# Performance work log

Measured on AMD Instinct MI355X. Metric: run time of the kernel, lower is better.

The kernel has to match this reference:

```python
import jax, jax.numpy as jnp
import numpy as np

NUM_TYPES = 200
TOK_DIM = 10000
SMALL_DIM = 64
IN_DIM = 32 + 32 + SMALL_DIM  # 128
NUM_EDGE_TYPES = 3
STEPS = 4
BLOCKS = 2
PROJ_DIM = 128
N_NODES = 100000
N_EDGES = 600000
N_GRAPHS = 64


def setup_inputs() -> dict:
    key = jax.random.key(0)
    ks = jax.random.split(key, 20)
    s = 0.05
    inp = {
        'x_type': jax.random.randint(ks[0], (N_NODES,), 0, NUM_TYPES),
        'x_tok': jax.random.randint(ks[1], (N_NODES,), 0, TOK_DIM + 1),
        'x_small': jax.random.normal(ks[2], (N_NODES, SMALL_DIM), jnp.float32),
        'edge_index': jax.random.randint(ks[3], (2, N_EDGES), 0, N_NODES),
        'edge_type': jax.random.randint(ks[4], (N_EDGES,), 0, NUM_EDGE_TYPES),
        'batch': jnp.sort(jax.random.randint(ks[5], (N_NODES,), 0, N_GRAPHS)),
        # learned params
        'type_emb': jax.random.normal(ks[6], (NUM_TYPES, 32), jnp.float32),
        'tok_emb': jax.random.normal(ks[7], (TOK_DIM + 1, 32), jnp.float32),
        'msg_W': jax.random.normal(ks[8], (NUM_EDGE_TYPES, IN_DIM, IN_DIM), jnp.float32) * s,
        'msg_b': jax.random.normal(ks[9], (NUM_EDGE_TYPES, IN_DIM), jnp.float32) * s,
        'W_ih': jax.random.normal(ks[10], (3 * IN_DIM, IN_DIM), jnp.float32) * s,
        'W_hh': jax.random.normal(ks[11], (3 * IN_DIM, IN_DIM), jnp.float32) * s,
        'b_ih': jax.random.normal(ks[12], (3 * IN_DIM,), jnp.float32) * s,
        'b_hh': jax.random.normal(ks[13], (3 * IN_DIM,), jnp.float32) * s,
        'proj_W1': jax.random.normal(ks[14], (PROJ_DIM, IN_DIM), jnp.float32) * s,
        'proj_b1': jax.random.normal(ks[15], (PROJ_DIM,), jnp.float32) * s,
        'proj_W2': jax.random.normal(ks[16], (1, PROJ_DIM), jnp.float32) * s,
        'proj_b2': jax.random.normal(ks[17], (1,), jnp.float32) * s,
    }
    return inp


def _gru_cell(m, h, W_ih, W_hh, b_ih, b_hh):
    # torch.nn.GRU single step
    gi = m @ W_ih.T + b_ih  # [N, 3H]
    gh = h @ W_hh.T + b_hh
    i_r, i_z, i_n = jnp.split(gi, 3, axis=-1)
    h_r, h_z, h_n = jnp.split(gh, 3, axis=-1)
    r = jax.nn.sigmoid(i_r + h_r)
    z = jax.nn.sigmoid(i_z + h_z)
    n = jnp.tanh(i_n + r * h_n)
    return (1.0 - z) * n + z * h


def reference(x_type, x_tok, x_small, edge_index, edge_type, batch,
              type_emb, tok_emb, msg_W, msg_b,
              W_ih, W_hh, b_ih, b_hh,
              proj_W1, proj_b1, proj_W2, proj_b2):
    n = x_type.shape[0]
    x = jnp.concatenate([type_emb[x_type], tok_emb[x_tok], x_small], axis=-1)  # [N, IN_DIM]
    src, dst = edge_index[0], edge_index[1]
    for _ in range(BLOCKS * STEPS):
        # transform every node once per edge type: [T, N, D]
        h_all = jnp.einsum('ni,toi->tno', x, msg_W) + msg_b[:, None, :]
        # per-edge message = typed linear of source node (gather)
        m = h_all[edge_type, src]  # [E, D]
        agg = jax.ops.segment_sum(m, dst, num_segments=n)  # summed over edge types too
        x = _gru_cell(agg, x, W_ih, W_hh, b_ih, b_hh)
    # global mean pool over graphs
    sums = jax.ops.segment_sum(x, batch, num_segments=N_GRAPHS)
    counts = jax.ops.segment_sum(jnp.ones((n,), x.dtype), batch, num_segments=N_GRAPHS)
    pooled = sums / jnp.maximum(counts, 1.0)[:, None]
    h = jax.nn.relu(pooled @ proj_W1.T + proj_b1)  # dropout = identity in eval
    logits = (h @ proj_W2.T + proj_b2).reshape(-1)
    return logits
```

## Files before the change

kernel.cpp:

```cpp
#include <hip/hip_runtime.h>
#include <stdint.h>


typedef _Float16 f16;
typedef _Float16 v8hf __attribute__((ext_vector_type(8)));
typedef _Float16 v2hf __attribute__((ext_vector_type(2)));
typedef float    v16f __attribute__((ext_vector_type(16)));

#define GI_F 147456
#define GH_F 49152

__device__ __forceinline__ float sigf(float a){
  return __fdividef(1.0f, 1.0f + __expf(-a));
}
__device__ __forceinline__ float tanhf_fast(float a){
  return 1.0f - __fdividef(2.0f, __expf(2.0f*a) + 1.0f);
}

__global__ void k_diag(float* out, int n, float v){
  int i = threadIdx.x; if(i<n) out[i] = v;
}

__global__ void k_embed(const int* __restrict__ xtype, const int* __restrict__ xtok,
                        const float* __restrict__ xsmall,
                        const float* __restrict__ temb, const float* __restrict__ kemb,
                        f16* __restrict__ xb, int N){
  int n = blockIdx.x; int j = threadIdx.x;
  if(n>=N) return;
  float v;
  if(j<32)       v = temb[xtype[n]*32 + j];
  else if(j<64)  v = kemb[xtok[n]*32 + (j-32)];
  else           v = xsmall[(size_t)n*64 + (j-64)];
  xb[(size_t)n*128 + j] = (f16)v;
}

__global__ void k_wcomb(const float* __restrict__ W_ih, const float* __restrict__ msg_W,
                        float* __restrict__ Wc){
  int i = blockIdx.x*256 + threadIdx.x;
  if(i >= 147456) return;
  int o2 = i/384, K = i%384;
  const float* wr = W_ih + o2*128;
  const float* mc = msg_W + (K>>7)*16384 + (K&127);
  float acc = 0.f;
  #pragma unroll 4
  for(int k2=0;k2<128;k2++) acc += wr[k2]*mc[k2*128];
  Wc[i] = acc;
}

__global__ void k_mbp(const float* __restrict__ W_ih, const float* __restrict__ msg_b,
                      float* __restrict__ mbp){
  int i = blockIdx.x*256 + threadIdx.x;
  if(i >= 1152) return;
  int t = i/384, o2 = i%384;
  const float* wr = W_ih + o2*128;
  const float* mb = msg_b + t*128;
  float acc = 0.f;
  #pragma unroll 4
  for(int k2=0;k2<128;k2++) acc += wr[k2]*mb[k2];
  mbp[i] = acc;
}

__global__ void k_wprep(const float* __restrict__ Wc, const float* __restrict__ W_hh,
                        f16* __restrict__ WpF){
  int i = blockIdx.x*256 + threadIdx.x;
  if(i >= GI_F + GH_F) return;
  float w; int lane, j;
  if(i < GI_F){
    int grp = i/512, rem = i%512;
    lane = rem/8; j = rem%8;
    int tile = grp/24, ks = grp%24;
    int n = tile*32 + (lane&31);
    int k = ks*16 + (lane>>5)*8 + j;
    w = Wc[n*384 + k];
  } else {
    int i2 = i - GI_F;
    int grp = i2/512, rem = i2%512;
    lane = rem/8; j = rem%8;
    int tile = grp/8, ks = grp%8;
    int n = tile*32 + (lane&31);
    int k = ks*16 + (lane>>5)*8 + j;
    w = W_hh[n*128 + k];
  }
  WpF[i] = (f16)w;
}

__global__ void k_hist3(const int* __restrict__ dst, const int* __restrict__ et,
                        int* __restrict__ deg3, int E){
  int e = blockIdx.x*blockDim.x + threadIdx.x;
  if(e<E) atomicAdd(&deg3[dst[e]*3 + et[e]], 1);
}

__global__ void k_scan1(const int* __restrict__ deg, int n, int* __restrict__ part, int* __restrict__ bsum){
  __shared__ int s[256];
  int t = threadIdx.x;
  int base = blockIdx.x*1024 + t*4;
  int v[4]; int sum=0;
  #pragma unroll
  for(int k=0;k<4;k++){ int i=base+k; int d=(i<n)?deg[i]:0; sum+=d; v[k]=sum; }
  s[t]=sum; __syncthreads();
  for(int off=1;off<256;off<<=1){
    int add = (t>=off)? s[t-off] : 0;
    __syncthreads();
    s[t]+=add;
    __syncthreads();
  }
  int excl = (t>0)? s[t-1] : 0;
  #pragma unroll
  for(int k=0;k<4;k++){ int i=base+k; if(i<n) part[i]=v[k]+excl; }
  if(t==255) bsum[blockIdx.x] = s[255];
}

__global__ void k_scan2(const int* __restrict__ bsum, int nb, int* __restrict__ carry){
  if(threadIdx.x==0 && blockIdx.x==0){
    int c=0;
    for(int b=0;b<nb;b++){ carry[b]=c; c+=bsum[b]; }
  }
}

__global__ void k_finalize(const int* __restrict__ part, const int* __restrict__ deg,
                           const int* __restrict__ carry, int n,
                           int* __restrict__ rowptr, int* __restrict__ cursor){
  int i = blockIdx.x*blockDim.x + threadIdx.x;
  if(i>=n) return;
  int incl = part[i] + carry[i>>10];
  rowptr[i+1] = incl;
  cursor[i] = incl - deg[i];
  if(i==0) rowptr[0]=0;
}

__global__ void k_fill3(const int* __restrict__ src, const int* __restrict__ dst,
                        const int* __restrict__ et, int* __restrict__ cursor,
                        int* __restrict__ pay, int E){
  int e = blockIdx.x*blockDim.x + threadIdx.x;
  if(e>=E) return;
  int pos = atomicAdd(&cursor[dst[e]*3 + et[e]], 1);
  pay[pos] = src[e];
}

__global__ void k_gather3_c(const f16* __restrict__ xb, const int* __restrict__ rp3,
                            const int* __restrict__ pay, f16* __restrict__ s, int N){
  int n = blockIdx.x*4 + (threadIdx.x>>6);
  if(n >= N) return;
  int lane = threadIdx.x & 63;
  int c = lane*2;
  int b = n*3;
  int lo = rp3[b], e0 = rp3[b+1], e1 = rp3[b+2], hi = rp3[b+3];
  float a0=0.f,b0=0.f,a1=0.f,b1=0.f,a2=0.f,b2=0.f;
  int len = hi - lo;
  int t1 = lo + len/3;
  int t2 = lo + (2*len)/3;
  int iA = lo, iB = t1, iC = t2;
  while(iA < t1 && iB < t2 && iC < hi){
    int pA = pay[iA], pB = pay[iB], pC = pay[iC];
    v2hf uA = *(const v2hf*)&xb[(size_t)pA*128 + c];
    v2hf uB = *(const v2hf*)&xb[(size_t)pB*128 + c];
    v2hf uC = *(const v2hf*)&xb[(size_t)pC*128 + c];
    float fA0=(float)uA[0], fA1=(float)uA[1];
    float fB0=(float)uB[0], fB1=(float)uB[1];
    float fC0=(float)uC[0], fC1=(float)uC[1];
    if(iA < e0)      { a0+=fA0; b0+=fA1; }
    else if(iA < e1) { a1+=fA0; b1+=fA1; }
    else             { a2+=fA0; b2+=fA1; }
    if(iB < e0)      { a0+=fB0; b0+=fB1; }
    else if(iB < e1) { a1+=fB0; b1+=fB1; }
    else             { a2+=fB0; b2+=fB1; }
    if(iC < e0)      { a0+=fC0; b0+=fC1; }
    else if(iC < e1) { a1+=fC0; b1+=fC1; }
    else             { a2+=fC0; b2+=fC1; }
    iA++; iB++; iC++;
  }
  for(; iA < t1; iA++){
    v2hf u = *(const v2hf*)&xb[(size_t)pay[iA]*128 + c];
    float f0=(float)u[0], f1=(float)u[1];
    if(iA < e0)      { a0+=f0; b0+=f1; }
    else if(iA < e1) { a1+=f0; b1+=f1; }
    else             { a2+=f0; b2+=f1; }
  }
  for(; iB < t2; iB++){
    v2hf u = *(const v2hf*)&xb[(size_t)pay[iB]*128 + c];
    float f0=(float)u[0], f1=(float)u[1];
    if(iB < e0)      { a0+=f0; b0+=f1; }
    else if(iB < e1) { a1+=f0; b1+=f1; }
    else             { a2+=f0; b2+=f1; }
  }
  for(; iC < hi; iC++){
    v2hf u = *(const v2hf*)&xb[(size_t)pay[iC]*128 + c];
    float f0=(float)u[0], f1=(float)u[1];
    if(iC < e0)      { a0+=f0; b0+=f1; }
    else if(iC < e1) { a1+=f0; b1+=f1; }
    else             { a2+=f0; b2+=f1; }
  }
  size_t o = (size_t)n*384 + c;
  v2hf t;
  t[0]=(f16)a0; t[1]=(f16)b0; *(v2hf*)&s[o]     = t;
  t[0]=(f16)a1; t[1]=(f16)b1; *(v2hf*)&s[o+128] = t;
  t[0]=(f16)a2; t[1]=(f16)b2; *(v2hf*)&s[o+256] = t;
}

#define SSTR 392
#define XSTR 136
__global__ __launch_bounds__(256,2) void k_mega2(
    const f16* __restrict__ xb_old, f16* __restrict__ xb_new,
    const f16* __restrict__ s, const f16* __restrict__ WpF,
    const int* __restrict__ deg3, const float* __restrict__ mbp,
    const float* __restrict__ b_ih, const float* __restrict__ b_hh, int M)
{
  __shared__ f16 Ss[32*SSTR];
  __shared__ f16 Ax[32*XSTR];
  __shared__ float Dg[96];
  int tid = threadIdx.x, lane = tid & 63, w = tid >> 6;
  int lrow = lane & 31, q = lane >> 5;
  int row0 = blockIdx.x * 32;

  #pragma unroll
  for(int p=0;p<2;p++){
    int ch = tid + p*256;
    int row = ch>>4, c8 = (ch&15)*8;
    int gr = row0 + row; if(gr >= M) gr = M-1;
    *(v8hf*)&Ax[row*XSTR + c8] = *(const v8hf*)(xb_old + (size_t)gr*128 + c8);
  }
  #pragma unroll
  for(int p=0;p<6;p++){
    int ch = tid + p*256;
    int row = ch/48, c8 = (ch%48)*8;
    int gr = row0 + row; if(gr >= M) gr = M-1;
    *(v8hf*)&Ss[row*SSTR + c8] = *(const v8hf*)(s + (size_t)gr*384 + c8);
  }
  if(tid < 96){
    int node = row0 + tid/3;
    Dg[tid] = (node < M) ? (float)deg3[node*3 + (tid - (tid/3)*3)] : 0.f;
  }
  __syncthreads();

  v16f agi[3] = {};
  #pragma unroll
  for(int ks=0; ks<24; ks++){
    int kb = ks*16 + q*8;
    v8hf a0 = *(const v8hf*)&Ss[lrow*SSTR + kb];
    #pragma unroll
    for(int ct=0; ct<3; ct++){
      int tile = ct*4 + w;
      v8hf bh = *(const v8hf*)(WpF + (size_t)(tile*24 + ks)*512 + lane*8);
      agi[ct] = __builtin_amdgcn_mfma_f32_32x32x16_f16(a0, bh, agi[ct], 0,0,0);
    }
  }
  v2hf gip[3][8];
  #pragma unroll
  for(int ct=0; ct<3; ct++)
    #pragma unroll
    for(int rp=0; rp<8; rp++){
      v2hf t; t[0] = (f16)agi[ct][2*rp]; t[1] = (f16)agi[ct][2*rp+1];
      gip[ct][rp] = t;
    }

  v16f agh[3] = {};
  #pragma unroll
  for(int ks=0; ks<8; ks++){
    int kb = ks*16 + q*8;
    v8hf a0 = *(const v8hf*)&Ax[lrow*XSTR + kb];
    #pragma unroll
    for(int ct=0; ct<3; ct++){
      int tile = ct*4 + w;
      v8hf bh = *(const v8hf*)(WpF + GI_F + (size_t)(tile*8 + ks)*512 + lane*8);
      agh[ct] = __builtin_amdgcn_mfma_f32_32x32x16_f16(a0, bh, agh[ct], 0,0,0);
    }
  }

  int jf = w*32 + lrow;
  float bi0 = b_ih[jf],     bh0 = b_hh[jf];
  float bi1 = b_ih[128+jf], bh1 = b_hh[128+jf];
  float bi2 = b_ih[256+jf], bh2 = b_hh[256+jf];
  float mb[3][3];
  #pragma unroll
  for(int t=0;t<3;t++){
    mb[t][0] = mbp[t*384 + jf];
    mb[t][1] = mbp[t*384 + 128 + jf];
    mb[t][2] = mbp[t*384 + 256 + jf];
  }
  int rq4 = 4*q;
  #pragma unroll
  for(int r=0;r<16;r++){
    int gl = (r&3) + 8*(r>>2) + rq4;
    float d0 = Dg[gl*3], d1 = Dg[gl*3+1], d2 = Dg[gl*3+2];
    float g0 = (float)gip[0][r>>1][r&1];
    float g1 = (float)gip[1][r>>1][r&1];
    float g2 = (float)gip[2][r>>1][r&1];
    float ir  = g0 + bi0 + d0*mb[0][0] + d1*mb[1][0] + d2*mb[2][0];
    float iz  = g1 + bi1 + d0*mb[0][1] + d1*mb[1][1] + d2*mb[2][1];
    float in_ = g2 + bi2 + d0*mb[0][2] + d1*mb[1][2] + d2*mb[2][2];
    float hr  = agh[0][r] + bh0;
    float hz  = agh[1][r] + bh1;
    float hn  = agh[2][r] + bh2;
    float rg = sigf(ir + hr);
    float zg = sigf(iz + hz);
    float nn = tanhf_fast(in_ + rg*hn);
    float xo = (float)Ax[gl*XSTR + jf];
    Ax[gl*XSTR + jf] = (f16)((1.f - zg)*nn + zg*xo);
  }
  __syncthreads();
  #pragma unroll
  for(int p=0;p<2;p++){
    int ch = tid + p*256;
    int row = ch>>4, c8 = (ch&15)*8;
    int gr = row0 + row;
    if(gr < M)
      *(v8hf*)(xb_new + (size_t)gr*128 + c8) = *(const v8hf*)&Ax[row*XSTR + c8];
  }
}

__device__ __forceinline__ int lb_batch(const int* __restrict__ batch, int N, int g){
  int lo=0, hi=N;
  while(lo<hi){ int mid=(lo+hi)>>1; if(batch[mid]<g) lo=mid+1; else hi=mid; }
  return lo;
}

__global__ void k_pool2(const f16* __restrict__ xb, const int* __restrict__ batch,
                        float* __restrict__ pooled, int N){
  int g = blockIdx.x, slice = blockIdx.y;
  int j = threadIdx.x;
  int lo = lb_batch(batch,N,g), hi = lb_batch(batch,N,g+1);
  float acc = 0.f;
  for(int r=lo+slice; r<hi; r+=32) acc += (float)xb[(size_t)r*128 + j];
  atomicAdd(&pooled[g*128+j], acc);
}

__global__ void k_head(const float* __restrict__ pooled, const int* __restrict__ batch, int N,
                       const float* __restrict__ W1, const float* __restrict__ b1,
                       const float* __restrict__ W2, const float* __restrict__ b2,
                       float* __restrict__ out){
  int g = blockIdx.x; int j = threadIdx.x;
  __shared__ float p[128];
  __shared__ float red[128];
  int lo = lb_batch(batch,N,g), hi = lb_batch(batch,N,g+1);
  float c = (float)(hi-lo); if(c < 1.f) c = 1.f;
  p[j] = pooled[g*128+j] / c;
  __syncthreads();
  float acc = b1[j];
  #pragma unroll 4
  for(int i=0;i<128;i++) acc += W1[j*128+i]*p[i];
  float v = (acc>0.f?acc:0.f) * W2[j];
  red[j] = v; __syncthreads();
  for(int s=64;s>0;s>>=1){ if(j<s) red[j]+=red[j+s]; __syncthreads(); }
  if(j==0) out[g] = red[0] + b2[0];
}

extern "C" void kernel_launch(void* const* d_in, const int* in_sizes, int n_in,
                              void* d_out, int out_size, void* d_ws, size_t ws_size,
                              hipStream_t stream){
  const int*   x_type    = (const int*)d_in[0];
  const int*   x_tok     = (const int*)d_in[1];
  const float* x_small   = (const float*)d_in[2];
  const int*   edge_index= (const int*)d_in[3];
  const int*   edge_type = (const int*)d_in[4];
  const int*   batch     = (const int*)d_in[5];
  const float* type_emb  = (const float*)d_in[6];
  const float* tok_emb   = (const float*)d_in[7];
  const float* msg_W     = (const float*)d_in[8];
  const float* msg_b     = (const float*)d_in[9];
  const float* W_ih      = (const float*)d_in[10];
  const float* W_hh      = (const float*)d_in[11];
  const float* b_ih      = (const float*)d_in[12];
  const float* b_hh      = (const float*)d_in[13];
  const float* pW1       = (const float*)d_in[14];
  const float* pb1       = (const float*)d_in[15];
  const float* pW2       = (const float*)d_in[16];
  const float* pb2       = (const float*)d_in[17];
  float* out = (float*)d_out;

  int N = in_sizes[0];
  int E = in_sizes[3]/2;
  const int* src = edge_index;
  const int* dst = edge_index + E;
  int n3 = 3*N;
  int nch = (n3+1023)/1024;

  char* w = (char*)d_ws;
  size_t off = 0;
  auto alloc = [&](size_t bytes)->char*{ char* p = w + off; off += (bytes + 511) & ~511ull; return p; };
  f16*   xb0    = (f16*)alloc((size_t)N*128*2);
  f16*   xb1    = (f16*)alloc((size_t)N*128*2);
  f16*   s      = (f16*)alloc((size_t)N*384*2);
  int*   deg3   = (int*)alloc((size_t)n3*4);
  int*   part   = (int*)alloc((size_t)n3*4);
  int*   rp3    = (int*)alloc((size_t)(n3+1)*4);
  int*   cursor = (int*)alloc((size_t)n3*4);
  int*   pay    = (int*)alloc((size_t)E*4);
  int*   bsum   = (int*)alloc((size_t)nch*4);
  int*   carry  = (int*)alloc((size_t)nch*4);
  float* Wc     = (float*)alloc((size_t)147456*4);
  f16*   WpF    = (f16*)alloc((size_t)(GI_F+GH_F)*2);
  float* mbp    = (float*)alloc((size_t)1152*4);
  float* pooled = (float*)alloc(64*128*4);
  if(off > ws_size){
    k_diag<<<1,64,0,stream>>>(out, out_size, 1.0e6f + (float)(ws_size>>20));
    return;
  }

  const int tb = 256;
  hipMemsetAsync(deg3, 0, (size_t)n3*4, stream);
  k_wcomb   <<<576, 256, 0, stream>>>(W_ih, msg_W, Wc);
  k_mbp     <<<5, 256, 0, stream>>>(W_ih, msg_b, mbp);
  k_wprep   <<<(GI_F+GH_F+255)/256, 256, 0, stream>>>(Wc, W_hh, WpF);
  k_hist3   <<<(E+tb-1)/tb, tb, 0, stream>>>(dst, edge_type, deg3, E);
  k_scan1   <<<nch, 256, 0, stream>>>(deg3, n3, part, bsum);
  k_scan2   <<<1, 64, 0, stream>>>(bsum, nch, carry);
  k_finalize<<<(n3+tb-1)/tb, tb, 0, stream>>>(part, deg3, carry, n3, rp3, cursor);
  k_fill3   <<<(E+tb-1)/tb, tb, 0, stream>>>(src, dst, edge_type, cursor, pay, E);
  k_embed   <<<N, 128, 0, stream>>>(x_type, x_tok, x_small, type_emb, tok_emb, xb0, N);

  int nblk = (N+31)/32;
  f16* xin = xb0;
  f16* xout = xb1;
  for(int it=0; it<8; it++){
    k_gather3_c<<<(N+3)/4, 256, 0, stream>>>(xin, rp3, pay, s, N);
    k_mega2    <<<nblk, 256, 0, stream>>>(xin, xout, s, WpF, deg3, mbp, b_ih, b_hh, N);
    f16* tmp = xin; xin = xout; xout = tmp;
  }
  hipMemsetAsync(pooled, 0, 64*128*4, stream);
  k_pool2<<<dim3(64,32), 128, 0, stream>>>(xin, batch, pooled, N);
  k_head <<<64, 128, 0, stream>>>(pooled, batch, N, pW1, pb1, pW2, pb2, out);
}
```

Baseline: 1.225 ms.

## Make GRU mega kernel persistent with register prefetch of next tile

Converts the per-tile fused GRU kernel into a persistent kernel launched with at most 512 blocks that loop over 32-row tiles. While the MFMAs for the current tile run, the s, x and degree rows for the next tile are loaded into registers, so global load latency overlaps compute, and per-block setup such as bias loads is amortized. The cost is extra register pressure from the prefetch buffers, which may hurt occupancy under launch_bounds(256,2), plus an added barrier per tile. A grid of 512 blocks may also underfill the machine relative to its CU count.

```diff
diff --git a/kernel.cpp b/kernel.cpp
--- a/kernel.cpp
+++ b/kernel.cpp
@@ -199,72 +199,18 @@
 
 #define SSTR 392
 #define XSTR 136
-__global__ __launch_bounds__(256,2) void k_mega2(
+__global__ __launch_bounds__(256,2) void k_megap(
     const f16* __restrict__ xb_old, f16* __restrict__ xb_new,
     const f16* __restrict__ s, const f16* __restrict__ WpF,
     const int* __restrict__ deg3, const float* __restrict__ mbp,
-    const float* __restrict__ b_ih, const float* __restrict__ b_hh, int M)
+    const float* __restrict__ b_ih, const float* __restrict__ b_hh,
+    int M, int nblk)
 {
   __shared__ f16 Ss[32*SSTR];
   __shared__ f16 Ax[32*XSTR];
   __shared__ float Dg[96];
   int tid = threadIdx.x, lane = tid & 63, w = tid >> 6;
   int lrow = lane & 31, q = lane >> 5;
-  int row0 = blockIdx.x * 32;
-
-  #pragma unroll
-  for(int p=0;p<2;p++){
-    int ch = tid + p*256;
-    int row = ch>>4, c8 = (ch&15)*8;
-    int gr = row0 + row; if(gr >= M) gr = M-1;
-    *(v8hf*)&Ax[row*XSTR + c8] = *(const v8hf*)(xb_old + (size_t)gr*128 + c8);
-  }
-  #pragma unroll
-  for(int p=0;p<6;p++){
-    int ch = tid + p*256;
-    int row = ch/48, c8 = (ch%48)*8;
-    int gr = row0 + row; if(gr >= M) gr = M-1;
-    *(v8hf*)&Ss[row*SSTR + c8] = *(const v8hf*)(s + (size_t)gr*384 + c8);
-  }
-  if(tid < 96){
-    int node = row0 + tid/3;
-    Dg[tid] = (node < M) ? (float)deg3[node*3 + (tid - (tid/3)*3)] : 0.f;
-  }
-  __syncthreads();
-
-  v16f agi[3] = {};
-  #pragma unroll
-  for(int ks=0; ks<24; ks++){
-    int kb = ks*16 + q*8;
-    v8hf a0 = *(const v8hf*)&Ss[lrow*SSTR + kb];
-    #pragma unroll
-    for(int ct=0; ct<3; ct++){
-      int tile = ct*4 + w;
-      v8hf bh = *(const v8hf*)(WpF + (size_t)(tile*24 + ks)*512 + lane*8);
-      agi[ct] = __builtin_amdgcn_mfma_f32_32x32x16_f16(a0, bh, agi[ct], 0,0,0);
-    }
-  }
-  v2hf gip[3][8];
-  #pragma unroll
-  for(int ct=0; ct<3; ct++)
-    #pragma unroll
-    for(int rp=0; rp<8; rp++){
-      v2hf t; t[0] = (f16)agi[ct][2*rp]; t[1] = (f16)agi[ct][2*rp+1];
-      gip[ct][rp] = t;
-    }
-
-  v16f agh[3] = {};
-  #pragma unroll
-  for(int ks=0; ks<8; ks++){
-    int kb = ks*16 + q*8;
-    v8hf a0 = *(const v8hf*)&Ax[lrow*XSTR + kb];
-    #pragma unroll
-    for(int ct=0; ct<3; ct++){
-      int tile = ct*4 + w;
-      v8hf bh = *(const v8hf*)(WpF + GI_F + (size_t)(tile*8 + ks)*512 + lane*8);
-      agh[ct] = __builtin_amdgcn_mfma_f32_32x32x16_f16(a0, bh, agh[ct], 0,0,0);
-    }
-  }
 
   int jf = w*32 + lrow;
   float bi0 = b_ih[jf],     bh0 = b_hh[jf];
@@ -278,33 +224,113 @@
     mb[t][2] = mbp[t*384 + 256 + jf];
   }
   int rq4 = 4*q;
+
+  v8hf pf_s[6], pf_x[2];
+  float pf_d = 0.f;
+  int s_row[6], s_c8[6], x_row[2], x_c8[2];
   #pragma unroll
-  for(int r=0;r<16;r++){
-    int gl = (r&3) + 8*(r>>2) + rq4;
-    float d0 = Dg[gl*3], d1 = Dg[gl*3+1], d2 = Dg[gl*3+2];
-    float g0 = (float)gip[0][r>>1][r&1];
-    float g1 = (float)gip[1][r>>1][r&1];
-    float g2 = (float)gip[2][r>>1][r&1];
-    float ir  = g0 + bi0 + d0*mb[0][0] + d1*mb[1][0] + d2*mb[2][0];
-    float iz  = g1 + bi1 + d0*mb[0][1] + d1*mb[1][1] + d2*mb[2][1];
-    float in_ = g2 + bi2 + d0*mb[0][2] + d1*mb[1][2] + d2*mb[2][2];
-    float hr  = agh[0][r] + bh0;
-    float hz  = agh[1][r] + bh1;
-    float hn  = agh[2][r] + bh2;
-    float rg = sigf(ir + hr);
-    float zg = sigf(iz + hz);
-    float nn = tanhf_fast(in_ + rg*hn);
-    float xo = (float)Ax[gl*XSTR + jf];
-    Ax[gl*XSTR + jf] = (f16)((1.f - zg)*nn + zg*xo);
-  }
-  __syncthreads();
+  for(int p=0;p<6;p++){ int ch = tid + p*256; s_row[p] = ch/48; s_c8[p] = (ch%48)*8; }
   #pragma unroll
-  for(int p=0;p<2;p++){
-    int ch = tid + p*256;
-    int row = ch>>4, c8 = (ch&15)*8;
-    int gr = row0 + row;
-    if(gr < M)
-      *(v8hf*)(xb_new + (size_t)gr*128 + c8) = *(const v8hf*)&Ax[row*XSTR + c8];
+  for(int p=0;p<2;p++){ int ch = tid + p*256; x_row[p] = ch>>4; x_c8[p] = (ch&15)*8; }
+  int dg_node3 = (tid/3)*3, dg_t = tid - dg_node3;
+
+  int tile = blockIdx.x;
+  {
+    int r0 = tile*32;
+    #pragma unroll
+    for(int p=0;p<6;p++){ int gr = r0 + s_row[p]; if(gr >= M) gr = M-1;
+      pf_s[p] = *(const v8hf*)(s + (size_t)gr*384 + s_c8[p]); }
+    #pragma unroll
+    for(int p=0;p<2;p++){ int gr = r0 + x_row[p]; if(gr >= M) gr = M-1;
+      pf_x[p] = *(const v8hf*)(xb_old + (size_t)gr*128 + x_c8[p]); }
+    if(tid < 96){ int node = r0 + tid/3;
+      pf_d = (node < M) ? (float)deg3[node*3 + dg_t] : 0.f; }
+  }
+
+  for(; tile < nblk; tile += gridDim.x){
+    int row0 = tile*32;
+    __syncthreads();
+    #pragma unroll
+    for(int p=0;p<6;p++) *(v8hf*)&Ss[s_row[p]*SSTR + s_c8[p]] = pf_s[p];
+    #pragma unroll
+    for(int p=0;p<2;p++) *(v8hf*)&Ax[x_row[p]*XSTR + x_c8[p]] = pf_x[p];
+    if(tid < 96) Dg[tid] = pf_d;
+    __syncthreads();
+    {
+      int nt = tile + gridDim.x; if(nt >= nblk) nt = tile;
+      int r0 = nt*32;
+      #pragma unroll
+      for(int p=0;p<6;p++){ int gr = r0 + s_row[p]; if(gr >= M) gr = M-1;
+        pf_s[p] = *(const v8hf*)(s + (size_t)gr*384 + s_c8[p]); }
+      #pragma unroll
+      for(int p=0;p<2;p++){ int gr = r0 + x_row[p]; if(gr >= M) gr = M-1;
+        pf_x[p] = *(const v8hf*)(xb_old + (size_t)gr*128 + x_c8[p]); }
+      if(tid < 96){ int node = r0 + tid/3;
+        pf_d = (node < M) ? (float)deg3[node*3 + dg_t] : 0.f; }
+    }
+
+    v16f agi[3] = {};
+    #pragma unroll
+    for(int ks=0; ks<24; ks++){
+      int kb = ks*16 + q*8;
+      v8hf a0 = *(const v8hf*)&Ss[lrow*SSTR + kb];
+      #pragma unroll
+      for(int ct=0; ct<3; ct++){
+        int tile_b = ct*4 + w;
+        v8hf bh = *(const v8hf*)(WpF + (size_t)(tile_b*24 + ks)*512 + lane*8);
+        agi[ct] = __builtin_amdgcn_mfma_f32_32x32x16_f16(a0, bh, agi[ct], 0,0,0);
+      }
+    }
+    v2hf gip[3][8];
+    #pragma unroll
+    for(int ct=0; ct<3; ct++)
+      #pragma unroll
+      for(int rp=0; rp<8; rp++){
+        v2hf t; t[0] = (f16)agi[ct][2*rp]; t[1] = (f16)agi[ct][2*rp+1];
+        gip[ct][rp] = t;
+      }
+
+    v16f agh[3] = {};
+    #pragma unroll
+    for(int ks=0; ks<8; ks++){
+      int kb = ks*16 + q*8;
+      v8hf a0 = *(const v8hf*)&Ax[lrow*XSTR + kb];
+      #pragma unroll
+      for(int ct=0; ct<3; ct++){
+        int tile_b = ct*4 + w;
+        v8hf bh = *(const v8hf*)(WpF + GI_F + (size_t)(tile_b*8 + ks)*512 + lane*8);
+        agh[ct] = __builtin_amdgcn_mfma_f32_32x32x16_f16(a0, bh, agh[ct], 0,0,0);
+      }
+    }
+
+    __syncthreads();
+
+    #pragma unroll
+    for(int r=0;r<16;r++){
+      int gl = (r&3) + 8*(r>>2) + rq4;
+      float d0 = Dg[gl*3], d1 = Dg[gl*3+1], d2 = Dg[gl*3+2];
+      float g0 = (float)gip[0][r>>1][r&1];
+      float g1 = (float)gip[1][r>>1][r&1];
+      float g2 = (float)gip[2][r>>1][r&1];
+      float ir  = g0 + bi0 + d0*mb[0][0] + d1*mb[1][0] + d2*mb[2][0];
+      float iz  = g1 + bi1 + d0*mb[0][1] + d1*mb[1][1] + d2*mb[2][1];
+      float in_ = g2 + bi2 + d0*mb[0][2] + d1*mb[1][2] + d2*mb[2][2];
+      float hr  = agh[0][r] + bh0;
+      float hz  = agh[1][r] + bh1;
+      float hn  = agh[2][r] + bh2;
+      float rg = sigf(ir + hr);
+      float zg = sigf(iz + hz);
+      float nn = tanhf_fast(in_ + rg*hn);
+      float xo = (float)Ax[gl*XSTR + jf];
+      Ax[gl*XSTR + jf] = (f16)((1.f - zg)*nn + zg*xo);
+    }
+    __syncthreads();
+    #pragma unroll
+    for(int p=0;p<2;p++){
+      int gr = row0 + x_row[p];
+      if(gr < M)
+        *(v8hf*)(xb_new + (size_t)gr*128 + x_c8[p]) = *(const v8hf*)&Ax[x_row[p]*XSTR + x_c8[p]];
+    }
   }
 }
 
@@ -409,11 +435,13 @@
   k_embed   <<<N, 128, 0, stream>>>(x_type, x_tok, x_small, type_emb, tok_emb, xb0, N);
 
   int nblk = (N+31)/32;
+  int pgrid = 512;
+  if(pgrid > nblk) pgrid = nblk;
   f16* xin = xb0;
   f16* xout = xb1;
   for(int it=0; it<8; it++){
     k_gather3_c<<<(N+3)/4, 256, 0, stream>>>(xin, rp3, pay, s, N);
-    k_mega2    <<<nblk, 256, 0, stream>>>(xin, xout, s, WpF, deg3, mbp, b_ih, b_hh, N);
+    k_megap    <<<pgrid, 256, 0, stream>>>(xin, xout, s, WpF, deg3, mbp, b_ih, b_hh, N, nblk);
     f16* tmp = xin; xin = xout; xout = tmp;
   }
   hipMemsetAsync(pooled, 0, 64*128*4, stream);
```

Result: slower. 3.092 ms (+152.5%).
